# Kernel optimization log

Measured on AMD Instinct MI355X. Metric: run time of the kernel, lower is better.

## Reference

```python
import jax, jax.numpy as jnp
import numpy as np
from jax import lax

HEAD_NUM = 16
QKV_DIM = 16
TOP_K = 2
SQRT_EMBED = 16.0   # sqrt_embedding_dim for E=256
LOGIT_CLIP = 10.0


def setup_inputs() -> dict:
    key = jax.random.key(0)
    ks = jax.random.split(key, 12)
    B, P, N1, E, HD, NE = 256, 100, 101, 256, 256, 8
    s = 0.05
    return {
        "encoded_last_node": jax.random.normal(ks[0], (B, P, E), jnp.float32),
        "attr": jax.random.uniform(ks[1], (B, P, 4), jnp.float32),
        "encoded_nodes": jax.random.normal(ks[2], (B, N1, E), jnp.float32),
        "ninf_mask": jnp.zeros((B, P, N1), jnp.float32),
        "attention_bias": jax.random.normal(ks[3], (B, P, N1), jnp.float32),
        "attention_bias1": jax.random.normal(ks[4], (B, P, N1), jnp.float32),
        "Wq_last": jax.random.normal(ks[5], (E + 4, HD), jnp.float32) * s,
        "Wk": jax.random.normal(ks[6], (E, HD), jnp.float32) * s,
        "Wv": jax.random.normal(ks[7], (E, HD), jnp.float32) * s,
        "Wg": jax.random.normal(ks[8], (HD, NE), jnp.float32) * s,
        "expert_W": jax.random.normal(ks[9], (NE, HD, E), jnp.float32) * s,
        "expert_b": jnp.zeros((NE, E), jnp.float32),
    }


def _heads(x, H, D):
    B, n, _ = x.shape
    return x.reshape(B, n, H, D).transpose(0, 2, 1, 3)  # (B,H,n,D)


def reference(encoded_last_node, attr, encoded_nodes, ninf_mask,
              attention_bias, attention_bias1, Wq_last, Wk, Wv,
              Wg, expert_W, expert_b):
    B, P, E = encoded_last_node.shape
    H, D = HEAD_NUM, QKV_DIM
    # q from [last_node ; attr], k/v from encoded_nodes (set_kv)
    q = _heads(jnp.concatenate([encoded_last_node, attr], axis=-1) @ Wq_last, H, D)
    k = _heads(encoded_nodes @ Wk, H, D)   # (B,H,N+1,D)
    v = _heads(encoded_nodes @ Wv, H, D)
    inv_sqrt_d = 1.0 / jnp.sqrt(jnp.asarray(D, jnp.float32))
    score = jnp.einsum('bhpd,bhnd->bhpn', q, k) * inv_sqrt_d
    score = score + ninf_mask[:, None, :, :]           # rank3 ninf mask
    w = jax.nn.softmax(score, axis=-1)
    out = jnp.einsum('bhpn,bhnd->bhpd', w, v)
    out_concat = out.transpose(0, 2, 1, 3).reshape(B, P, H * D)
    # --- top-k gated MoE combine (node-level routing, eval path) ---
    x = out_concat.reshape(B * P, H * D)               # tokens
    logits = x @ Wg                                    # (T, NE)
    top_v, top_i = lax.top_k(logits, TOP_K)
    top_g = jax.nn.softmax(top_v, axis=-1)
    gates = jnp.zeros_like(logits).at[
        jnp.arange(x.shape[0])[:, None], top_i].set(top_g)   # (T, NE)
    expert_out = jnp.einsum('tf,efo->teo', x, expert_W) + expert_b[None]
    mh = jnp.einsum('teo,te->to', expert_out, gates).reshape(B, P, E)
    # --- single-head pointer scores with bias + tanh clipping ---
    score2 = jnp.einsum('bpe,bne->bpn', mh, encoded_nodes)
    score2 = score2 + attention_bias + attention_bias1
    score2 = LOGIT_CLIP * jnp.tanh(score2 / SQRT_EMBED)
    probs = jax.nn.softmax(score2 + ninf_mask, axis=-1)  # (B,P,N+1)
    return probs
```

## Files before the change

### kernel.cpp

```cpp
#include <hip/hip_runtime.h>
#include <hip/hip_bf16.h>

#define B   256
#define P   100
#define N1  101
#define E   256
#define HD  256
#define H   16
#define D   16
#define NE  8
#define NTOK (B*P)
#define NKV  (B*N1)
#define NCHK 200
#define CHKSZ 128

typedef __attribute__((ext_vector_type(8))) short short8;
typedef __attribute__((ext_vector_type(4))) float f32x4;
typedef unsigned short ushort_t;

__device__ __forceinline__ unsigned short f2bf(float f) {
  unsigned int u = __float_as_uint(f);
  unsigned int r = (u + 0x7fffu + ((u >> 16) & 1u)) >> 16;
  return (unsigned short)r;
}
__device__ __forceinline__ float bf2f(unsigned short b) {
  return __uint_as_float(((unsigned int)b) << 16);
}
__device__ __forceinline__ unsigned int cvtpk(float a, float b) {
  unsigned int r;
  asm("v_cvt_pk_bf16_f32 %0, %1, %2" : "=v"(r) : "v"(a), "v"(b));
  return r;
}
__device__ __forceinline__ float lo2f(unsigned int u) {
  return __uint_as_float(u << 16);
}
__device__ __forceinline__ float hi2f(unsigned int u) {
  return __uint_as_float(u & 0xffff0000u);
}

__device__ __forceinline__ void split3_pack(const float* v, uint4& uh,
                                            uint4& um, uint4& ul) {
  unsigned int hw[4], mw[4], lw[4];
#pragma unroll
  for (int jj = 0; jj < 4; ++jj) {
    float va = v[2 * jj], vb = v[2 * jj + 1];
    unsigned int h = cvtpk(va, vb);
    float ra = va - lo2f(h), rb = vb - hi2f(h);
    unsigned int m = cvtpk(ra, rb);
    float sa = ra - lo2f(m), sb = rb - hi2f(m);
    unsigned int l = cvtpk(sa, sb);
    hw[jj] = h; mw[jj] = m; lw[jj] = l;
  }
  uh.x = hw[0]; uh.y = hw[1]; uh.z = hw[2]; uh.w = hw[3];
  um.x = mw[0]; um.y = mw[1]; um.z = mw[2]; um.w = mw[3];
  ul.x = lw[0]; ul.y = lw[1]; ul.z = lw[2]; ul.w = lw[3];
}

__device__ __forceinline__ void wsplit3_body(const float* __restrict__ W,
                                             uint4* __restrict__ Wp, int Kreal,
                                             int gid) {
  const int lane = gid & 63;
  const int rest = gid >> 6;
  const int gct = rest & 15;
  const int kt = rest >> 4;
  const int k0 = kt * 32 + (lane >> 4) * 8;
  const int c = gct * 16 + (lane & 15);
  float v[8];
#pragma unroll
  for (int j = 0; j < 8; ++j) {
    int kk = k0 + j;
    v[j] = (kk < Kreal) ? W[(size_t)kk * 256 + c] : 0.f;
  }
  uint4 uh, um, ul;
  split3_pack(v, uh, um, ul);
  Wp[(size_t)(rest * 3 + 0) * 64 + lane] = uh;
  Wp[(size_t)(rest * 3 + 1) * 64 + lane] = um;
  Wp[(size_t)(rest * 3 + 2) * 64 + lane] = ul;
}

__global__ __launch_bounds__(256) void prep_kernel(
    const float* __restrict__ eW, uint4* __restrict__ Wp,
    const float* __restrict__ Wk, uint4* __restrict__ Wk3,
    const float* __restrict__ Wv, uint4* __restrict__ Wv3,
    const float* __restrict__ Wq, uint4* __restrict__ Wq3) {
  const int bx = blockIdx.x;
  const int tid = threadIdx.x;
  if (bx < 256) {
    const int gid = bx * 256 + tid;
    const int lane = gid & 63;
    const int rest = gid >> 6;
    const int gct = rest & 15;
    const int kt = (rest >> 4) & 7;
    const int e = rest >> 7;
    const int kbase = kt * 32 + (lane >> 4) * 8;
    const int c = gct * 16 + (lane & 15);
    unsigned int hi[4], lo[4];
#pragma unroll
    for (int jj = 0; jj < 4; ++jj) {
      float v0 = eW[((size_t)e * HD + (kbase + 2 * jj)) * E + c];
      float v1 = eW[((size_t)e * HD + (kbase + 2 * jj + 1)) * E + c];
      unsigned int h = cvtpk(v0, v1);
      float r0 = v0 - lo2f(h), r1 = v1 - hi2f(h);
      unsigned int l = cvtpk(r0, r1);
      hi[jj] = h; lo[jj] = l;
    }
    uint4 uh, ul;
    uh.x = hi[0]; uh.y = hi[1]; uh.z = hi[2]; uh.w = hi[3];
    ul.x = lo[0]; ul.y = lo[1]; ul.z = lo[2]; ul.w = lo[3];
    Wp[(size_t)(rest * 2 + 0) * 64 + lane] = uh;
    Wp[(size_t)(rest * 2 + 1) * 64 + lane] = ul;
  } else if (bx < 288) {
    wsplit3_body(Wk, Wk3, 256, (bx - 256) * 256 + tid);
  } else if (bx < 320) {
    wsplit3_body(Wv, Wv3, 256, (bx - 288) * 256 + tid);
  } else {
    wsplit3_body(Wq, Wq3, 260, (bx - 320) * 256 + tid);
  }
}

__global__ __launch_bounds__(256) void kvproj3_kernel(
    const float* __restrict__ enc, const uint4* __restrict__ Wk3,
    const uint4* __restrict__ Wv3, float* __restrict__ kout,
    float* __restrict__ vout) {
  const int KT = 8;
  const int NKG = KT * 4;
  const int RSTRIDE = KT * 12 + 1;
  __shared__ uint4 als[32 * 97];
  const int tid = threadIdx.x;
  const int row0 = blockIdx.x * 32;
  for (int i = tid; i < 32 * NKG; i += 256) {
    const int row = i >> 5;
    const int kg = i & 31;
    float v[8];
    const float4* s = (const float4*)(enc + (size_t)(row0 + row) * 256 + kg * 8);
    float4 x0 = s[0], x1 = s[1];
    v[0] = x0.x; v[1] = x0.y; v[2] = x0.z; v[3] = x0.w;
    v[4] = x1.x; v[5] = x1.y; v[6] = x1.z; v[7] = x1.w;
    uint4 uh, um, ul;
    split3_pack(v, uh, um, ul);
    const int slot = row * RSTRIDE + kg;
    als[slot] = uh;
    als[slot + NKG] = um;
    als[slot + 2 * NKG] = ul;
  }
  __syncthreads();
  const int w = tid >> 6;
  const int lane = tid & 63;
  const int lr = lane & 15;
  const int lg4 = lane >> 4;
  f32x4 acck[2][4], accv[2][4];
#pragma unroll
  for (int rt = 0; rt < 2; ++rt)
#pragma unroll
    for (int ct = 0; ct < 4; ++ct) {
      acck[rt][ct] = (f32x4){0.f, 0.f, 0.f, 0.f};
      accv[rt][ct] = (f32x4){0.f, 0.f, 0.f, 0.f};
    }
  for (int kt = 0; kt < KT; ++kt) {
    short8 ah[2], am[2], al[2];
#pragma unroll
    for (int rt = 0; rt < 2; ++rt) {
      const int base = (rt * 16 + lr) * RSTRIDE + kt * 4 + lg4;
      ah[rt] = __builtin_bit_cast(short8, als[base]);
      am[rt] = __builtin_bit_cast(short8, als[base + NKG]);
      al[rt] = __builtin_bit_cast(short8, als[base + 2 * NKG]);
    }
#pragma unroll
    for (int ct = 0; ct < 4; ++ct) {
      const int gct = w * 4 + ct;
      const size_t base = (size_t)((kt * 16 + gct) * 3) * 64 + lane;
      {
        short8 bh = __builtin_bit_cast(short8, Wk3[base]);
        short8 bm = __builtin_bit_cast(short8, Wk3[base + 64]);
        short8 bl = __builtin_bit_cast(short8, Wk3[base + 128]);
#pragma unroll
        for (int rt = 0; rt < 2; ++rt) {
          f32x4 a = acck[rt][ct];
          a = __builtin_amdgcn_mfma_f32_16x16x32_bf16(ah[rt], bh, a, 0, 0, 0);
          a = __builtin_amdgcn_mfma_f32_16x16x32_bf16(ah[rt], bm, a, 0, 0, 0);
          a = __builtin_amdgcn_mfma_f32_16x16x32_bf16(am[rt], bh, a, 0, 0, 0);
          a = __builtin_amdgcn_mfma_f32_16x16x32_bf16(am[rt], bm, a, 0, 0, 0);
          a = __builtin_amdgcn_mfma_f32_16x16x32_bf16(ah[rt], bl, a, 0, 0, 0);
          a = __builtin_amdgcn_mfma_f32_16x16x32_bf16(al[rt], bh, a, 0, 0, 0);
          acck[rt][ct] = a;
        }
      }
      {
        short8 bh = __builtin_bit_cast(short8, Wv3[base]);
        short8 bm = __builtin_bit_cast(short8, Wv3[base + 64]);
        short8 bl = __builtin_bit_cast(short8, Wv3[base + 128]);
#pragma unroll
        for (int rt = 0; rt < 2; ++rt) {
          f32x4 a = accv[rt][ct];
          a = __builtin_amdgcn_mfma_f32_16x16x32_bf16(ah[rt], bh, a, 0, 0, 0);
          a = __builtin_amdgcn_mfma_f32_16x16x32_bf16(ah[rt], bm, a, 0, 0, 0);
          a = __builtin_amdgcn_mfma_f32_16x16x32_bf16(am[rt], bh, a, 0, 0, 0);
          a = __builtin_amdgcn_mfma_f32_16x16x32_bf16(am[rt], bm, a, 0, 0, 0);
          a = __builtin_amdgcn_mfma_f32_16x16x32_bf16(ah[rt], bl, a, 0, 0, 0);
          a = __builtin_amdgcn_mfma_f32_16x16x32_bf16(al[rt], bh, a, 0, 0, 0);
          accv[rt][ct] = a;
        }
      }
    }
  }
#pragma unroll
  for (int rt = 0; rt < 2; ++rt) {
#pragma unroll
    for (int ct = 0; ct < 4; ++ct) {
      const int gct = w * 4 + ct;
#pragma unroll
      for (int reg = 0; reg < 4; ++reg) {
        const int row = row0 + rt * 16 + lg4 * 4 + reg;
        int bb = row / N1, nn = row - bb * N1;
        size_t o = (((size_t)bb * H + gct) * N1 + nn) * D + lr;
        kout[o] = acck[rt][ct][reg];
        vout[o] = accv[rt][ct][reg];
      }
    }
  }
}

template <int KT, int MODE>
__global__ __launch_bounds__(256) void proj3_kernel(
    const float* __restrict__ src, const float* __restrict__ attr,
    const uint4* __restrict__ Wp3, float* __restrict__ outp) {
  const int RSTRIDE = KT * 12 + 1;
  __shared__ uint4 als[32 * (KT * 12 + 1)];
  const int tid = threadIdx.x;
  const int row0 = blockIdx.x * 32;
  const int NKG = KT * 4;
  for (int i = tid; i < 32 * NKG; i += 256) {
    const int row = i / NKG;
    const int kg = i - row * NKG;
    float v[8];
    const int kbase = kg * 8;
    if (MODE == 0 || kbase < 256) {
      const float4* s = (const float4*)(src + (size_t)(row0 + row) * 256 + kbase);
      float4 x0 = s[0], x1 = s[1];
      v[0] = x0.x; v[1] = x0.y; v[2] = x0.z; v[3] = x0.w;
      v[4] = x1.x; v[5] = x1.y; v[6] = x1.z; v[7] = x1.w;
    } else {
#pragma unroll
      for (int j = 0; j < 8; ++j) {
        int k = kbase + j;
        v[j] = (k >= 256 && k < 260) ? attr[(size_t)(row0 + row) * 4 + (k - 256)]
                                     : 0.f;
      }
    }
    uint4 uh, um, ul;
    split3_pack(v, uh, um, ul);
    const int slot = row * RSTRIDE + kg;
    als[slot] = uh;
    als[slot + NKG] = um;
    als[slot + 2 * NKG] = ul;
  }
  __syncthreads();
  const int w = tid >> 6;
  const int lane = tid & 63;
  const int lr = lane & 15;
  const int lg4 = lane >> 4;
  f32x4 acc[2][4];
#pragma unroll
  for (int rt = 0; rt < 2; ++rt)
#pragma unroll
    for (int ct = 0; ct < 4; ++ct) acc[rt][ct] = (f32x4){0.f, 0.f, 0.f, 0.f};
  for (int kt = 0; kt < KT; ++kt) {
    short8 ah[2], am[2], al[2];
#pragma unroll
    for (int rt = 0; rt < 2; ++rt) {
      const int base = (rt * 16 + lr) * RSTRIDE + kt * 4 + lg4;
      ah[rt] = __builtin_bit_cast(short8, als[base]);
      am[rt] = __builtin_bit_cast(short8, als[base + NKG]);
      al[rt] = __builtin_bit_cast(short8, als[base + 2 * NKG]);
    }
#pragma unroll
    for (int ct = 0; ct < 4; ++ct) {
      const int gct = w * 4 + ct;
      const size_t base = (size_t)((kt * 16 + gct) * 3) * 64 + lane;
      short8 bh = __builtin_bit_cast(short8, Wp3[base]);
      short8 bm = __builtin_bit_cast(short8, Wp3[base + 64]);
      short8 bl = __builtin_bit_cast(short8, Wp3[base + 128]);
#pragma unroll
      for (int rt = 0; rt < 2; ++rt) {
        f32x4 a = acc[rt][ct];
        a = __builtin_amdgcn_mfma_f32_16x16x32_bf16(ah[rt], bh, a, 0, 0, 0);
        a = __builtin_amdgcn_mfma_f32_16x16x32_bf16(ah[rt], bm, a, 0, 0, 0);
        a = __builtin_amdgcn_mfma_f32_16x16x32_bf16(am[rt], bh, a, 0, 0, 0);
        a = __builtin_amdgcn_mfma_f32_16x16x32_bf16(am[rt], bm, a, 0, 0, 0);
        a = __builtin_amdgcn_mfma_f32_16x16x32_bf16(ah[rt], bl, a, 0, 0, 0);
        a = __builtin_amdgcn_mfma_f32_16x16x32_bf16(al[rt], bh, a, 0, 0, 0);
        acc[rt][ct] = a;
      }
    }
  }
#pragma unroll
  for (int rt = 0; rt < 2; ++rt) {
#pragma unroll
    for (int ct = 0; ct < 4; ++ct) {
      const int gct = w * 4 + ct;
#pragma unroll
      for (int reg = 0; reg < 4; ++reg) {
        const int row = row0 + rt * 16 + lg4 * 4 + reg;
        size_t o;
        if (MODE == 0) {
          int bb = row / N1, nn = row - bb * N1;
          o = (((size_t)bb * H + gct) * N1 + nn) * D + lr;
        } else {
          int bb = row / P, pp = row - bb * P;
          o = (((size_t)bb * H + gct) * P + pp) * D + lr;
        }
        outp[o] = acc[rt][ct][reg];
      }
    }
  }
}

__device__ __forceinline__ float dot16f(
    const float4& a0, const float4& a1, const float4& a2, const float4& a3,
    const float4& b0, const float4& b1, const float4& b2, const float4& b3) {
  float s = a0.x * b0.x;
  s = fmaf(a0.y, b0.y, s); s = fmaf(a0.z, b0.z, s); s = fmaf(a0.w, b0.w, s);
  s = fmaf(a1.x, b1.x, s); s = fmaf(a1.y, b1.y, s); s = fmaf(a1.z, b1.z, s);
  s = fmaf(a1.w, b1.w, s);
  s = fmaf(a2.x, b2.x, s); s = fmaf(a2.y, b2.y, s); s = fmaf(a2.z, b2.z, s);
  s = fmaf(a2.w, b2.w, s);
  s = fmaf(a3.x, b3.x, s); s = fmaf(a3.y, b3.y, s); s = fmaf(a3.z, b3.z, s);
  s = fmaf(a3.w, b3.w, s);
  return s;
}

__global__ __launch_bounds__(256) void attn_kernel(
    const float* __restrict__ q, const float* __restrict__ k,
    const float* __restrict__ v, const float* __restrict__ ninf,
    float* __restrict__ x) {
  const int b = blockIdx.x >> 3;
  const int h0 = (blockIdx.x & 7) * 2;
  __shared__ float4 kl4[2 * 208];
  __shared__ float4 vl4[2 * 208];
  const int tid = threadIdx.x;
  const int w = tid >> 6;
  const int lane = tid & 63;
  const int hh = w >> 1;
  const int h = h0 + hh;
  const int prow = (w & 1) * 64 + lane;
  const bool act = (prow < P);
  const int p = act ? prow : (P - 1);
  const float LOG2E = 1.4426950408889634f;
  const float c1 = 0.25f * LOG2E;
  const float* qb = q + (((size_t)b * H + h) * P + p) * D;
  float4 qa0 = *(const float4*)&qb[0];
  float4 qa1 = *(const float4*)&qb[4];
  float4 qa2 = *(const float4*)&qb[8];
  float4 qa3 = *(const float4*)&qb[12];
  qa0.x *= c1; qa0.y *= c1; qa0.z *= c1; qa0.w *= c1;
  qa1.x *= c1; qa1.y *= c1; qa1.z *= c1; qa1.w *= c1;
  qa2.x *= c1; qa2.y *= c1; qa2.z *= c1; qa2.w *= c1;
  qa3.x *= c1; qa3.y *= c1; qa3.z *= c1; qa3.w *= c1;
  const float* mrow = ninf + ((size_t)b * P + p) * N1;
  const float* kw = (const float*)(kl4 + hh * 208);
  const float* vw = (const float*)(vl4 + hh * 208);

  float m2 = -1e30f, l = 0.f;
  float o[16];
#pragma unroll
  for (int d = 0; d < 16; ++d) o[d] = 0.f;

#pragma unroll
  for (int ch = 0; ch < 2; ++ch) {
    const int c0 = ch ? 52 : 0;
    const int len = ch ? 49 : 52;
    const int nf4 = len * 4;
    __syncthreads();
    for (int i = tid; i < 2 * nf4; i += 256) {
      int hs = i / nf4, rem = i - hs * nf4;
      const float4* ks =
          (const float4*)(k + (((size_t)b * H + h0 + hs) * N1 + c0) * D);
      const float4* vs =
          (const float4*)(v + (((size_t)b * H + h0 + hs) * N1 + c0) * D);
      kl4[hs * 208 + rem] = ks[rem];
      vl4[hs * 208 + rem] = vs[rem];
    }
    __syncthreads();
    const int nit = len >> 2;
    float4 mk = *(const float4*)&mrow[c0];
    for (int it = 0; it < nit; ++it) {
      const int j = it * 4;
      const int nn = (it < nit - 1) ? (c0 + j + 4) : c0;
      float4 nx = *(const float4*)&mrow[nn];
      const float4* kr0 = (const float4*)&kw[(j + 0) * D];
      const float4* kr1 = (const float4*)&kw[(j + 1) * D];
      const float4* kr2 = (const float4*)&kw[(j + 2) * D];
      const float4* kr3 = (const float4*)&kw[(j + 3) * D];
      float4 k00 = kr0[0], k01 = kr0[1], k02 = kr0[2], k03 = kr0[3];
      float4 k10 = kr1[0], k11 = kr1[1], k12 = kr1[2], k13 = kr1[3];
      float4 k20 = kr2[0], k21 = kr2[1], k22 = kr2[2], k23 = kr2[3];
      float4 k30 = kr3[0], k31 = kr3[1], k32 = kr3[2], k33 = kr3[3];
      float s0 = fmaf(mk.x, LOG2E, dot16f(qa0, qa1, qa2, qa3, k00, k01, k02, k03));
      float s1 = fmaf(mk.y, LOG2E, dot16f(qa0, qa1, qa2, qa3, k10, k11, k12, k13));
      float s2 = fmaf(mk.z, LOG2E, dot16f(qa0, qa1, qa2, qa3, k20, k21, k22, k23));
      float s3 = fmaf(mk.w, LOG2E, dot16f(qa0, qa1, qa2, qa3, k30, k31, k32, k33));
      float gm = fmaxf(fmaxf(s0, s1), fmaxf(s2, s3));
      const float4* vr0 = (const float4*)&vw[(j + 0) * D];
      const float4* vr1 = (const float4*)&vw[(j + 1) * D];
      const float4* vr2 = (const float4*)&vw[(j + 2) * D];
      const float4* vr3 = (const float4*)&vw[(j + 3) * D];
      if (__any(gm > m2 + 8.f)) {
        float mn = fmaxf(gm, m2);
        float sc = exp2f(m2 - mn);
        float p0 = exp2f(s0 - mn), p1 = exp2f(s1 - mn);
        float p2 = exp2f(s2 - mn), p3 = exp2f(s3 - mn);
        l = fmaf(l, sc, (p0 + p1) + (p2 + p3));
#pragma unroll
        for (int dq = 0; dq < 4; ++dq) {
          float4 v0 = vr0[dq], v1 = vr1[dq], v2 = vr2[dq], v3 = vr3[dq];
          o[4 * dq + 0] = fmaf(o[4 * dq + 0], sc,
              fmaf(p0, v0.x, fmaf(p1, v1.x, fmaf(p2, v2.x, p3 * v3.x))));
          o[4 * dq + 1] = fmaf(o[4 * dq + 1], sc,
              fmaf(p0, v0.y, fmaf(p1, v1.y, fmaf(p2, v2.y, p3 * v3.y))));
          o[4 * dq + 2] = fmaf(o[4 * dq + 2], sc,
              fmaf(p0, v0.z, fmaf(p1, v1.z, fmaf(p2, v2.z, p3 * v3.z))));
          o[4 * dq + 3] = fmaf(o[4 * dq + 3], sc,
              fmaf(p0, v0.w, fmaf(p1, v1.w, fmaf(p2, v2.w, p3 * v3.w))));
        }
        m2 = mn;
      } else {
        float p0 = exp2f(s0 - m2), p1 = exp2f(s1 - m2);
        float p2 = exp2f(s2 - m2), p3 = exp2f(s3 - m2);
        l += (p0 + p1) + (p2 + p3);
#pragma unroll
        for (int dq = 0; dq < 4; ++dq) {
          float4 v0 = vr0[dq], v1 = vr1[dq], v2 = vr2[dq], v3 = vr3[dq];
          o[4 * dq + 0] = fmaf(p0, v0.x,
              fmaf(p1, v1.x, fmaf(p2, v2.x, fmaf(p3, v3.x, o[4 * dq + 0]))));
          o[4 * dq + 1] = fmaf(p0, v0.y,
              fmaf(p1, v1.y, fmaf(p2, v2.y, fmaf(p3, v3.y, o[4 * dq + 1]))));
          o[4 * dq + 2] = fmaf(p0, v0.z,
              fmaf(p1, v1.z, fmaf(p2, v2.z, fmaf(p3, v3.z, o[4 * dq + 2]))));
          o[4 * dq + 3] = fmaf(p0, v0.w,
              fmaf(p1, v1.w, fmaf(p2, v2.w, fmaf(p3, v3.w, o[4 * dq + 3]))));
        }
      }
      mk = nx;
    }
  }
  {
    const float tm = mrow[100];
    const float4* kr = (const float4*)&kw[48 * D];
    float4 k0 = kr[0], k1 = kr[1], k2 = kr[2], k3 = kr[3];
    float s = fmaf(tm, LOG2E, dot16f(qa0, qa1, qa2, qa3, k0, k1, k2, k3));
    float mn = fmaxf(m2, s);
    float sc = exp2f(m2 - mn);
    float pp = exp2f(s - mn);
    l = fmaf(l, sc, pp);
    const float4* vr = (const float4*)&vw[48 * D];
#pragma unroll
    for (int dq = 0; dq < 4; ++dq) {
      float4 v0 = vr[dq];
      o[4 * dq + 0] = fmaf(o[4 * dq + 0], sc, pp * v0.x);
      o[4 * dq + 1] = fmaf(o[4 * dq + 1], sc, pp * v0.y);
      o[4 * dq + 2] = fmaf(o[4 * dq + 2], sc, pp * v0.z);
      o[4 * dq + 3] = fmaf(o[4 * dq + 3], sc, pp * v0.w);
    }
  }
  if (act) {
    const float inv = 1.f / l;
    float* xr = &x[((size_t)b * P + p) * HD + h * D];
#pragma unroll
    for (int dq = 0; dq < 4; ++dq) {
      float4 t;
      t.x = o[4 * dq + 0] * inv; t.y = o[4 * dq + 1] * inv;
      t.z = o[4 * dq + 2] * inv; t.w = o[4 * dq + 3] * inv;
      *(float4*)&xr[4 * dq] = t;
    }
  }
}

__global__ __launch_bounds__(256) void logits_top2_kernel(
    const float* __restrict__ x, const float* __restrict__ Wg,
    int* __restrict__ topi, float* __restrict__ topg,
    ushort_t* __restrict__ xsplit) {
  __shared__ float xl[32][260];
  __shared__ float wgt[8 * 260];
  __shared__ float lg[32][9];
  const int tid = threadIdx.x;
  const int t0 = blockIdx.x * 32;
  for (int r = 0; r < 32; ++r) {
    float val = x[(size_t)(t0 + r) * HD + tid];
    xl[r][tid] = val;
    unsigned short hi = f2bf(val);
    unsigned short lo = f2bf(val - bf2f(hi));
    xsplit[(size_t)(t0 + r) * 512 + tid] = hi;
    xsplit[(size_t)(t0 + r) * 512 + 256 + tid] = lo;
  }
  for (int i = tid; i < E * NE; i += 256) {
    wgt[(i & 7) * 260 + (i >> 3)] = Wg[i];
  }
  __syncthreads();
  const int r = tid >> 3, e = tid & 7;
  float acc = 0.f;
  const float* xr = &xl[r][0];
  const float* wr = &wgt[e * 260];
  for (int f = 0; f < E; f += 4) {
    float4 xv = *(const float4*)&xr[f];
    float4 wv = *(const float4*)&wr[f];
    acc += xv.x * wv.x;
    acc += xv.y * wv.y;
    acc += xv.z * wv.z;
    acc += xv.w * wv.w;
  }
  lg[r][e] = acc;
  __syncthreads();
  if (tid < 32) {
    float v[8];
#pragma unroll
    for (int j = 0; j < 8; ++j) v[j] = lg[tid][j];
    int i1 = 0; float v1 = v[0];
#pragma unroll
    for (int j = 1; j < 8; ++j) if (v[j] > v1) { v1 = v[j]; i1 = j; }
    int i2 = -1; float v2 = -1e30f;
#pragma unroll
    for (int j = 0; j < 8; ++j)
      if (j != i1 && v[j] > v2) { v2 = v[j]; i2 = j; }
    float ex = __expf(v2 - v1);
    float g1 = 1.f / (1.f + ex);
    float g2 = ex / (1.f + ex);
    int t = t0 + tid;
    topi[t * 2 + 0] = i1; topi[t * 2 + 1] = i2;
    topg[t * 2 + 0] = g1; topg[t * 2 + 1] = g2;
  }
}

__global__ __launch_bounds__(CHKSZ) void moe_count_kernel(
    const int* __restrict__ topi, int* __restrict__ chunk_cnt) {
  __shared__ int cnt[NE];
  const int tid = threadIdx.x;
  if (tid < NE) cnt[tid] = 0;
  __syncthreads();
  const int t = blockIdx.x * CHKSZ + tid;
  atomicAdd(&cnt[topi[t * 2 + 0]], 1);
  atomicAdd(&cnt[topi[t * 2 + 1]], 1);
  __syncthreads();
  if (tid < NE) chunk_cnt[blockIdx.x * NE + tid] = cnt[tid];
}

__global__ __launch_bounds__(64) void moe_scan_kernel(
    const int* __restrict__ chunk_cnt, int* __restrict__ chunk_base,
    int* __restrict__ counts) {
  const int e = threadIdx.x;
  if (e < NE) {
    int run = 0;
    for (int c = 0; c < NCHK; ++c) {
      chunk_base[c * NE + e] = run;
      run += chunk_cnt[c * NE + e];
    }
    counts[e] = run;
  }
}

__global__ __launch_bounds__(CHKSZ) void moe_scatter_kernel(
    const int* __restrict__ topi, const float* __restrict__ topg,
    const int* __restrict__ chunk_base, int* __restrict__ list_tok,
    float* __restrict__ list_gate) {
  __shared__ int w0cnt[NE];
  const int tid = threadIdx.x;
  const int wv = tid >> 6, lane = tid & 63;
  const int t = blockIdx.x * CHKSZ + tid;
  const int ia = topi[t * 2 + 0], ib = topi[t * 2 + 1];
  const float ga = topg[t * 2 + 0], gb = topg[t * 2 + 1];
  const unsigned long long lmask = (lane == 0) ? 0ull : ((~0ull) >> (64 - lane));
  int prefA = 0, prefB = 0;
#pragma unroll
  for (int e = 0; e < NE; ++e) {
    unsigned long long mc = __ballot(ia == e) | __ballot(ib == e);
    if (wv == 0 && lane == 0) w0cnt[e] = __popcll(mc);
    int pref = __popcll(mc & lmask);
    if (ia == e) prefA = pref;
    if (ib == e) prefB = pref;
  }
  __syncthreads();
  const int baseA =
      chunk_base[blockIdx.x * NE + ia] + (wv ? w0cnt[ia] : 0) + prefA;
  const int baseB =
      chunk_base[blockIdx.x * NE + ib] + (wv ? w0cnt[ib] : 0) + prefB;
  list_tok[ia * NTOK + baseA] = (t << 1) | 0;
  list_gate[ia * NTOK + baseA] = ga;
  list_tok[ib * NTOK + baseB] = (t << 1) | 1;
  list_gate[ib * NTOK + baseB] = gb;
}

__global__ __launch_bounds__(256) void expert_gemm_kernel(
    const ushort_t* __restrict__ xsplit, const uint4* __restrict__ Wp,
    const float* __restrict__ eb, const int* __restrict__ list_tok,
    const float* __restrict__ list_gate, const int* __restrict__ counts,
    float* __restrict__ p0, float* __restrict__ p1) {
  int e = 0, t0 = -1;
  {
    int rem = blockIdx.x;
    for (int i = 0; i < NE; ++i) {
      int nt = (counts[i] + 47) / 48;
      if (rem < nt) { e = i; t0 = rem * 48; break; }
      rem -= nt;
    }
  }
  if (t0 < 0) return;
  const int cnt = counts[e];
  const int nr = min(48, cnt - t0);
  __shared__ uint4 xls[48 * 65];
  __shared__ int stok[48];
  __shared__ float sg[48];
  const int tid = threadIdx.x;
  if (tid < 48) {
    int src = e * NTOK + t0 + ((tid < nr) ? tid : 0);
    stok[tid] = list_tok[src];
    sg[tid] = (tid < nr) ? list_gate[e * NTOK + t0 + tid] : 0.f;
  }
  __syncthreads();
  for (int i = tid; i < 48 * 64; i += 256) {
    int r = i >> 6, ch = i & 63;
    const uint4* src = (const uint4*)(xsplit + (size_t)(stok[r] >> 1) * 512);
    xls[r * 65 + ch] = src[ch];
  }
  __syncthreads();
  const int w = tid >> 6;
  const int lane = tid & 63;
  const int lr = lane & 15;
  const int lg4 = lane >> 4;
  f32x4 acc[3][4];
#pragma unroll
  for (int rt = 0; rt < 3; ++rt)
#pragma unroll
    for (int ct = 0; ct < 4; ++ct) acc[rt][ct] = (f32x4){0.f, 0.f, 0.f, 0.f};

  for (int kt = 0; kt < 8; ++kt) {
    short8 afrag[3][2];
#pragma unroll
    for (int rt = 0; rt < 3; ++rt)
#pragma unroll
      for (int pl = 0; pl < 2; ++pl) {
        uint4 u = xls[(rt * 16 + lr) * 65 + pl * 32 + kt * 4 + lg4];
        afrag[rt][pl] = __builtin_bit_cast(short8, u);
      }
#pragma unroll
    for (int ct = 0; ct < 4; ++ct) {
      const int gct = w * 4 + ct;
      const size_t base = (size_t)(((e * 8 + kt) * 16 + gct) * 2) * 64 + lane;
      short8 bh = __builtin_bit_cast(short8, Wp[base]);
      short8 bl = __builtin_bit_cast(short8, Wp[base + 64]);
#pragma unroll
      for (int rt = 0; rt < 3; ++rt) {
        acc[rt][ct] = __builtin_amdgcn_mfma_f32_16x16x32_bf16(
            afrag[rt][0], bh, acc[rt][ct], 0, 0, 0);
        acc[rt][ct] = __builtin_amdgcn_mfma_f32_16x16x32_bf16(
            afrag[rt][0], bl, acc[rt][ct], 0, 0, 0);
        acc[rt][ct] = __builtin_amdgcn_mfma_f32_16x16x32_bf16(
            afrag[rt][1], bh, acc[rt][ct], 0, 0, 0);
      }
    }
  }
#pragma unroll
  for (int rt = 0; rt < 3; ++rt) {
#pragma unroll
    for (int ct = 0; ct < 4; ++ct) {
      const int col = (w * 4 + ct) * 16 + lr;
      const float bias = eb[e * E + col];
#pragma unroll
      for (int reg = 0; reg < 4; ++reg) {
        const int ridx = rt * 16 + lg4 * 4 + reg;
        if (ridx < nr) {
          const int tokw = stok[ridx];
          const float g = sg[ridx];
          float* dst = ((tokw & 1) ? p1 : p0) + (size_t)(tokw >> 1) * E + col;
          *dst = g * (acc[rt][ct][reg] + bias);
        }
      }
    }
  }
}

__global__ __launch_bounds__(256) void score2_fused_kernel(
    const float* __restrict__ p0, const float* __restrict__ p1,
    const float* __restrict__ enc, const float* __restrict__ ab,
    const float* __restrict__ ab1, const float* __restrict__ ninf,
    float* __restrict__ out) {
  const int b = blockIdx.x >> 1;
  const int half = blockIdx.x & 1;
  const int r0 = half * 50;
  __shared__ float4 mh4[50 * 64];
  const int tid = threadIdx.x;
  for (int i = tid; i < 50 * 64; i += 256) {
    int r = i >> 6, c4 = i & 63;
    size_t idx = (size_t)(b * P + r0 + r) * 64 + c4;
    float4 a = ((const float4*)p0)[idx];
    float4 c = ((const float4*)p1)[idx];
    float4 s;
    s.x = a.x + c.x; s.y = a.y + c.y; s.z = a.z + c.z; s.w = a.w + c.w;
    mh4[i] = s;
  }
  __syncthreads();
  const int w = tid >> 6;
  const int lane = tid & 63;
  const int n0 = lane;
  const int n1v = lane + 64;
  const bool has1 = (n1v < N1);
  const int n1 = has1 ? n1v : (N1 - 1);
  const float4* er0 = (const float4*)(enc + ((size_t)b * N1 + n0) * E);
  const float4* er1 = (const float4*)(enc + ((size_t)b * N1 + n1) * E);
  float acc0[13], acc1[13];
#pragma unroll
  for (int j = 0; j < 13; ++j) { acc0[j] = 0.f; acc1[j] = 0.f; }
  for (int kk = 0; kk < 64; ++kk) {
    float4 e0 = er0[kk];
    float4 e1 = er1[kk];
#pragma unroll
    for (int j = 0; j < 13; ++j) {
      const int r = w + j * 4;
      if (r < 50) {
        float4 mv = mh4[r * 64 + kk];
        acc0[j] = fmaf(mv.w, e0.w,
                  fmaf(mv.z, e0.z, fmaf(mv.y, e0.y, fmaf(mv.x, e0.x, acc0[j]))));
        acc1[j] = fmaf(mv.w, e1.w,
                  fmaf(mv.z, e1.z, fmaf(mv.y, e1.y, fmaf(mv.x, e1.x, acc1[j]))));
      }
    }
  }
#pragma unroll
  for (int j = 0; j < 13; ++j) {
    const int r = w + j * 4;
    if (r < 50) {
      const int prow = b * P + r0 + r;
      const float* arow = ab + (size_t)prow * N1;
      const float* a1row = ab1 + (size_t)prow * N1;
      const float* nrow = ninf + (size_t)prow * N1;
      float s0 = acc0[j] + arow[n0] + a1row[n0];
      float e20 = __expf(s0 * 0.125f);
      float v0 = 10.f - 20.f / (e20 + 1.f) + nrow[n0];
      float v1 = -1e30f;
      if (has1) {
        float s1 = acc1[j] + arow[n1v] + a1row[n1v];
        float e21 = __expf(s1 * 0.125f);
        v1 = 10.f - 20.f / (e21 + 1.f) + nrow[n1v];
      }
      float mx = fmaxf(v0, v1);
#pragma unroll
      for (int off = 32; off > 0; off >>= 1)
        mx = fmaxf(mx, __shfl_xor(mx, off, 64));
      float q0 = __expf(v0 - mx);
      float q1 = has1 ? __expf(v1 - mx) : 0.f;
      float sum = q0 + q1;
#pragma unroll
      for (int off = 32; off > 0; off >>= 1)
        sum += __shfl_xor(sum, off, 64);
      float inv = 1.f / sum;
      float* orow = out + (size_t)prow * N1;
      orow[n0] = q0 * inv;
      if (has1) orow[n1v] = q1 * inv;
    }
  }
}

extern "C" void kernel_launch(void* const* d_in, const int* in_sizes, int n_in,
                              void* d_out, int out_size, void* d_ws,
                              size_t ws_size, hipStream_t stream) {
  const float* eln  = (const float*)d_in[0];
  const float* attr = (const float*)d_in[1];
  const float* enc  = (const float*)d_in[2];
  const float* ninf = (const float*)d_in[3];
  const float* ab   = (const float*)d_in[4];
  const float* ab1  = (const float*)d_in[5];
  const float* Wq   = (const float*)d_in[6];
  const float* Wk   = (const float*)d_in[7];
  const float* Wv   = (const float*)d_in[8];
  const float* Wg   = (const float*)d_in[9];
  const float* eW   = (const float*)d_in[10];
  const float* eb   = (const float*)d_in[11];
  float* out = (float*)d_out;

  char* ws = (char*)d_ws;
  size_t off = 0;
  auto carve = [&](size_t bytes) {
    char* p = ws + off;
    off += (bytes + 255) & ~size_t(255);
    return p;
  };
  float* kbuf = (float*)carve(sizeof(float) * NKV * HD);
  float* vbuf = (float*)carve(sizeof(float) * NKV * HD);
  float* qbuf = (float*)carve(sizeof(float) * NTOK * HD);
  float* xbuf = (float*)carve(sizeof(float) * NTOK * HD);
  int*   topi = (int*)carve(sizeof(int) * NTOK * 2);
  float* topg = (float*)carve(sizeof(float) * NTOK * 2);
  int*   counts = (int*)carve(sizeof(int) * 16);
  int*   chunk_cnt = (int*)carve(sizeof(int) * NCHK * NE);
  int*   chunk_base = (int*)carve(sizeof(int) * NCHK * NE);
  int*   list_tok = (int*)carve(sizeof(int) * NE * NTOK);
  float* list_gate = (float*)carve(sizeof(float) * NE * NTOK);
  uint4* Wp  = (uint4*)carve(sizeof(ushort_t) * NE * HD * E * 2);
  uint4* Wk3 = (uint4*)carve((size_t)8 * 16 * 3 * 64 * 16);
  uint4* Wv3 = (uint4*)carve((size_t)8 * 16 * 3 * 64 * 16);
  uint4* Wq3 = (uint4*)carve((size_t)9 * 16 * 3 * 64 * 16);
  float* pp0 = kbuf;
  float* pp1 = vbuf;
  ushort_t* xsplit = (ushort_t*)qbuf;

  prep_kernel<<<356, 256, 0, stream>>>(eW, Wp, Wk, Wk3, Wv, Wv3, Wq, Wq3);
  kvproj3_kernel<<<NKV / 32, 256, 0, stream>>>(enc, Wk3, Wv3, kbuf, vbuf);
  proj3_kernel<9, 1><<<NTOK / 32, 256, 0, stream>>>(eln, attr, Wq3, qbuf);
  attn_kernel<<<B * 8, 256, 0, stream>>>(qbuf, kbuf, vbuf, ninf, xbuf);
  logits_top2_kernel<<<NTOK / 32, 256, 0, stream>>>(xbuf, Wg, topi, topg,
                                                    xsplit);
  moe_count_kernel<<<NCHK, CHKSZ, 0, stream>>>(topi, chunk_cnt);
  moe_scan_kernel<<<1, 64, 0, stream>>>(chunk_cnt, chunk_base, counts);
  moe_scatter_kernel<<<NCHK, CHKSZ, 0, stream>>>(topi, topg, chunk_base,
                                                 list_tok, list_gate);
  expert_gemm_kernel<<<1075, 256, 0, stream>>>(xsplit, Wp, eb, list_tok,
                                               list_gate, counts, pp0, pp1);
  score2_fused_kernel<<<512, 256, 0, stream>>>(pp0, pp1, enc, ab, ab1, ninf,
                                               out);
}
```

Measured before the change: 298.2 us.

## Process two query rows per thread in attention, four heads per block

The attention kernel now assigns one head per wavefront and two query rows per lane, so each block handles four heads and the grid is halved. Each K/V row read from LDS is reused for two queries, and the wasted half-wave of inactive rows is removed. The lazy-rescale branch with __any is replaced by an unconditional online-softmax rescale. In exchange, register pressure roughly doubles for accumulators, there are fewer blocks, and every step now pays extra exp2 and multiply work for the rescale.

```diff
diff --git a/kernel.cpp b/kernel.cpp
--- a/kernel.cpp
+++ b/kernel.cpp
@@ -333,37 +333,45 @@
     const float* __restrict__ q, const float* __restrict__ k,
     const float* __restrict__ v, const float* __restrict__ ninf,
     float* __restrict__ x) {
-  const int b = blockIdx.x >> 3;
-  const int h0 = (blockIdx.x & 7) * 2;
-  __shared__ float4 kl4[2 * 208];
-  __shared__ float4 vl4[2 * 208];
+  const int b = blockIdx.x >> 2;
+  const int h0 = (blockIdx.x & 3) * 4;
+  __shared__ float4 kl4[4 * 208];
+  __shared__ float4 vl4[4 * 208];
   const int tid = threadIdx.x;
   const int w = tid >> 6;
   const int lane = tid & 63;
-  const int hh = w >> 1;
-  const int h = h0 + hh;
-  const int prow = (w & 1) * 64 + lane;
-  const bool act = (prow < P);
-  const int p = act ? prow : (P - 1);
+  const int h = h0 + w;
+  const int p0 = lane;
+  const bool r1 = (lane + 64 < P);
+  const int p1 = r1 ? (lane + 64) : (P - 1);
   const float LOG2E = 1.4426950408889634f;
   const float c1 = 0.25f * LOG2E;
-  const float* qb = q + (((size_t)b * H + h) * P + p) * D;
-  float4 qa0 = *(const float4*)&qb[0];
-  float4 qa1 = *(const float4*)&qb[4];
-  float4 qa2 = *(const float4*)&qb[8];
-  float4 qa3 = *(const float4*)&qb[12];
+  const float* qbase = q + (((size_t)b * H + h) * P) * D;
+  float4 qa0 = *(const float4*)&qbase[p0 * D + 0];
+  float4 qa1 = *(const float4*)&qbase[p0 * D + 4];
+  float4 qa2 = *(const float4*)&qbase[p0 * D + 8];
+  float4 qa3 = *(const float4*)&qbase[p0 * D + 12];
+  float4 qb0 = *(const float4*)&qbase[p1 * D + 0];
+  float4 qb1 = *(const float4*)&qbase[p1 * D + 4];
+  float4 qb2 = *(const float4*)&qbase[p1 * D + 8];
+  float4 qb3 = *(const float4*)&qbase[p1 * D + 12];
   qa0.x *= c1; qa0.y *= c1; qa0.z *= c1; qa0.w *= c1;
   qa1.x *= c1; qa1.y *= c1; qa1.z *= c1; qa1.w *= c1;
   qa2.x *= c1; qa2.y *= c1; qa2.z *= c1; qa2.w *= c1;
   qa3.x *= c1; qa3.y *= c1; qa3.z *= c1; qa3.w *= c1;
-  const float* mrow = ninf + ((size_t)b * P + p) * N1;
-  const float* kw = (const float*)(kl4 + hh * 208);
-  const float* vw = (const float*)(vl4 + hh * 208);
-
-  float m2 = -1e30f, l = 0.f;
-  float o[16];
-#pragma unroll
-  for (int d = 0; d < 16; ++d) o[d] = 0.f;
+  qb0.x *= c1; qb0.y *= c1; qb0.z *= c1; qb0.w *= c1;
+  qb1.x *= c1; qb1.y *= c1; qb1.z *= c1; qb1.w *= c1;
+  qb2.x *= c1; qb2.y *= c1; qb2.z *= c1; qb2.w *= c1;
+  qb3.x *= c1; qb3.y *= c1; qb3.z *= c1; qb3.w *= c1;
+  const float* m0 = ninf + ((size_t)b * P + p0) * N1;
+  const float* m1 = ninf + ((size_t)b * P + p1) * N1;
+  const float* kw = (const float*)(kl4 + w * 208);
+  const float* vw = (const float*)(vl4 + w * 208);
+
+  float mA = -1e30f, mB = -1e30f, lA = 0.f, lB = 0.f;
+  float oA[16], oB[16];
+#pragma unroll
+  for (int d = 0; d < 16; ++d) { oA[d] = 0.f; oB[d] = 0.f; }
 
 #pragma unroll
   for (int ch = 0; ch < 2; ++ch) {
@@ -371,7 +379,7 @@
     const int len = ch ? 49 : 52;
     const int nf4 = len * 4;
     __syncthreads();
-    for (int i = tid; i < 2 * nf4; i += 256) {
+    for (int i = tid; i < 4 * nf4; i += 256) {
       int hs = i / nf4, rem = i - hs * nf4;
       const float4* ks =
           (const float4*)(k + (((size_t)b * H + h0 + hs) * N1 + c0) * D);
@@ -382,11 +390,13 @@
     }
     __syncthreads();
     const int nit = len >> 2;
-    float4 mk = *(const float4*)&mrow[c0];
+    float4 mk0 = *(const float4*)&m0[c0];
+    float4 mk1 = *(const float4*)&m1[c0];
     for (int it = 0; it < nit; ++it) {
       const int j = it * 4;
       const int nn = (it < nit - 1) ? (c0 + j + 4) : c0;
-      float4 nx = *(const float4*)&mrow[nn];
+      float4 nx0 = *(const float4*)&m0[nn];
+      float4 nx1 = *(const float4*)&m1[nn];
       const float4* kr0 = (const float4*)&kw[(j + 0) * D];
       const float4* kr1 = (const float4*)&kw[(j + 1) * D];
       const float4* kr2 = (const float4*)&kw[(j + 2) * D];
@@ -395,82 +405,97 @@
       float4 k10 = kr1[0], k11 = kr1[1], k12 = kr1[2], k13 = kr1[3];
       float4 k20 = kr2[0], k21 = kr2[1], k22 = kr2[2], k23 = kr2[3];
       float4 k30 = kr3[0], k31 = kr3[1], k32 = kr3[2], k33 = kr3[3];
-      float s0 = fmaf(mk.x, LOG2E, dot16f(qa0, qa1, qa2, qa3, k00, k01, k02, k03));
-      float s1 = fmaf(mk.y, LOG2E, dot16f(qa0, qa1, qa2, qa3, k10, k11, k12, k13));
-      float s2 = fmaf(mk.z, LOG2E, dot16f(qa0, qa1, qa2, qa3, k20, k21, k22, k23));
-      float s3 = fmaf(mk.w, LOG2E, dot16f(qa0, qa1, qa2, qa3, k30, k31, k32, k33));
-      float gm = fmaxf(fmaxf(s0, s1), fmaxf(s2, s3));
+      float sA0 = fmaf(mk0.x, LOG2E, dot16f(qa0, qa1, qa2, qa3, k00, k01, k02, k03));
+      float sA1 = fmaf(mk0.y, LOG2E, dot16f(qa0, qa1, qa2, qa3, k10, k11, k12, k13));
+      float sA2 = fmaf(mk0.z, LOG2E, dot16f(qa0, qa1, qa2, qa3, k20, k21, k22, k23));
+      float sA3 = fmaf(mk0.w, LOG2E, dot16f(qa0, qa1, qa2, qa3, k30, k31, k32, k33));
+      float sB0 = fmaf(mk1.x, LOG2E, dot16f(qb0, qb1, qb2, qb3, k00, k01, k02, k03));
+      float sB1 = fmaf(mk1.y, LOG2E, dot16f(qb0, qb1, qb2, qb3, k10, k11, k12, k13));
+      float sB2 = fmaf(mk1.z, LOG2E, dot16f(qb0, qb1, qb2, qb3, k20, k21, k22, k23));
+      float sB3 = fmaf(mk1.w, LOG2E, dot16f(qb0, qb1, qb2, qb3, k30, k31, k32, k33));
+      float mnA = fmaxf(fmaxf(fmaxf(sA0, sA1), fmaxf(sA2, sA3)), mA);
+      float mnB = fmaxf(fmaxf(fmaxf(sB0, sB1), fmaxf(sB2, sB3)), mB);
+      float scA = exp2f(mA - mnA);
+      float scB = exp2f(mB - mnB);
+      float pA0 = exp2f(sA0 - mnA), pA1 = exp2f(sA1 - mnA);
+      float pA2 = exp2f(sA2 - mnA), pA3 = exp2f(sA3 - mnA);
+      float pB0 = exp2f(sB0 - mnB), pB1 = exp2f(sB1 - mnB);
+      float pB2 = exp2f(sB2 - mnB), pB3 = exp2f(sB3 - mnB);
+      lA = fmaf(lA, scA, (pA0 + pA1) + (pA2 + pA3));
+      lB = fmaf(lB, scB, (pB0 + pB1) + (pB2 + pB3));
       const float4* vr0 = (const float4*)&vw[(j + 0) * D];
       const float4* vr1 = (const float4*)&vw[(j + 1) * D];
       const float4* vr2 = (const float4*)&vw[(j + 2) * D];
       const float4* vr3 = (const float4*)&vw[(j + 3) * D];
-      if (__any(gm > m2 + 8.f)) {
-        float mn = fmaxf(gm, m2);
-        float sc = exp2f(m2 - mn);
-        float p0 = exp2f(s0 - mn), p1 = exp2f(s1 - mn);
-        float p2 = exp2f(s2 - mn), p3 = exp2f(s3 - mn);
-        l = fmaf(l, sc, (p0 + p1) + (p2 + p3));
-#pragma unroll
-        for (int dq = 0; dq < 4; ++dq) {
-          float4 v0 = vr0[dq], v1 = vr1[dq], v2 = vr2[dq], v3 = vr3[dq];
-          o[4 * dq + 0] = fmaf(o[4 * dq + 0], sc,
-              fmaf(p0, v0.x, fmaf(p1, v1.x, fmaf(p2, v2.x, p3 * v3.x))));
-          o[4 * dq + 1] = fmaf(o[4 * dq + 1], sc,
-              fmaf(p0, v0.y, fmaf(p1, v1.y, fmaf(p2, v2.y, p3 * v3.y))));
-          o[4 * dq + 2] = fmaf(o[4 * dq + 2], sc,
-              fmaf(p0, v0.z, fmaf(p1, v1.z, fmaf(p2, v2.z, p3 * v3.z))));
-          o[4 * dq + 3] = fmaf(o[4 * dq + 3], sc,
-              fmaf(p0, v0.w, fmaf(p1, v1.w, fmaf(p2, v2.w, p3 * v3.w))));
-        }
-        m2 = mn;
-      } else {
-        float p0 = exp2f(s0 - m2), p1 = exp2f(s1 - m2);
-        float p2 = exp2f(s2 - m2), p3 = exp2f(s3 - m2);
-        l += (p0 + p1) + (p2 + p3);
-#pragma unroll
-        for (int dq = 0; dq < 4; ++dq) {
-          float4 v0 = vr0[dq], v1 = vr1[dq], v2 = vr2[dq], v3 = vr3[dq];
-          o[4 * dq + 0] = fmaf(p0, v0.x,
-              fmaf(p1, v1.x, fmaf(p2, v2.x, fmaf(p3, v3.x, o[4 * dq + 0]))));
-          o[4 * dq + 1] = fmaf(p0, v0.y,
-              fmaf(p1, v1.y, fmaf(p2, v2.y, fmaf(p3, v3.y, o[4 * dq + 1]))));
-          o[4 * dq + 2] = fmaf(p0, v0.z,
-              fmaf(p1, v1.z, fmaf(p2, v2.z, fmaf(p3, v3.z, o[4 * dq + 2]))));
-          o[4 * dq + 3] = fmaf(p0, v0.w,
-              fmaf(p1, v1.w, fmaf(p2, v2.w, fmaf(p3, v3.w, o[4 * dq + 3]))));
-        }
-      }
-      mk = nx;
+#pragma unroll
+      for (int dq = 0; dq < 4; ++dq) {
+        float4 v0 = vr0[dq], v1 = vr1[dq], v2 = vr2[dq], v3 = vr3[dq];
+        oA[4 * dq + 0] = fmaf(oA[4 * dq + 0], scA,
+            fmaf(pA0, v0.x, fmaf(pA1, v1.x, fmaf(pA2, v2.x, pA3 * v3.x))));
+        oA[4 * dq + 1] = fmaf(oA[4 * dq + 1], scA,
+            fmaf(pA0, v0.y, fmaf(pA1, v1.y, fmaf(pA2, v2.y, pA3 * v3.y))));
+        oA[4 * dq + 2] = fmaf(oA[4 * dq + 2], scA,
+            fmaf(pA0, v0.z, fmaf(pA1, v1.z, fmaf(pA2, v2.z, pA3 * v3.z))));
+        oA[4 * dq + 3] = fmaf(oA[4 * dq + 3], scA,
+            fmaf(pA0, v0.w, fmaf(pA1, v1.w, fmaf(pA2, v2.w, pA3 * v3.w))));
+        oB[4 * dq + 0] = fmaf(oB[4 * dq + 0], scB,
+            fmaf(pB0, v0.x, fmaf(pB1, v1.x, fmaf(pB2, v2.x, pB3 * v3.x))));
+        oB[4 * dq + 1] = fmaf(oB[4 * dq + 1], scB,
+            fmaf(pB0, v0.y, fmaf(pB1, v1.y, fmaf(pB2, v2.y, pB3 * v3.y))));
+        oB[4 * dq + 2] = fmaf(oB[4 * dq + 2], scB,
+            fmaf(pB0, v0.z, fmaf(pB1, v1.z, fmaf(pB2, v2.z, pB3 * v3.z))));
+        oB[4 * dq + 3] = fmaf(oB[4 * dq + 3], scB,
+            fmaf(pB0, v0.w, fmaf(pB1, v1.w, fmaf(pB2, v2.w, pB3 * v3.w))));
+      }
+      mA = mnA; mB = mnB;
+      mk0 = nx0; mk1 = nx1;
     }
   }
   {
-    const float tm = mrow[100];
+    const float tm0 = m0[100], tm1 = m1[100];
     const float4* kr = (const float4*)&kw[48 * D];
     float4 k0 = kr[0], k1 = kr[1], k2 = kr[2], k3 = kr[3];
-    float s = fmaf(tm, LOG2E, dot16f(qa0, qa1, qa2, qa3, k0, k1, k2, k3));
-    float mn = fmaxf(m2, s);
-    float sc = exp2f(m2 - mn);
-    float pp = exp2f(s - mn);
-    l = fmaf(l, sc, pp);
+    float sA = fmaf(tm0, LOG2E, dot16f(qa0, qa1, qa2, qa3, k0, k1, k2, k3));
+    float sB = fmaf(tm1, LOG2E, dot16f(qb0, qb1, qb2, qb3, k0, k1, k2, k3));
+    float mnA = fmaxf(mA, sA), mnB = fmaxf(mB, sB);
+    float scA = exp2f(mA - mnA), scB = exp2f(mB - mnB);
+    float pA = exp2f(sA - mnA), pB = exp2f(sB - mnB);
+    lA = fmaf(lA, scA, pA);
+    lB = fmaf(lB, scB, pB);
     const float4* vr = (const float4*)&vw[48 * D];
 #pragma unroll
     for (int dq = 0; dq < 4; ++dq) {
       float4 v0 = vr[dq];
-      o[4 * dq + 0] = fmaf(o[4 * dq + 0], sc, pp * v0.x);
-      o[4 * dq + 1] = fmaf(o[4 * dq + 1], sc, pp * v0.y);
-      o[4 * dq + 2] = fmaf(o[4 * dq + 2], sc, pp * v0.z);
-      o[4 * dq + 3] = fmaf(o[4 * dq + 3], sc, pp * v0.w);
-    }
-  }
-  if (act) {
-    const float inv = 1.f / l;
-    float* xr = &x[((size_t)b * P + p) * HD + h * D];
+      oA[4 * dq + 0] = fmaf(oA[4 * dq + 0], scA, pA * v0.x);
+      oA[4 * dq + 1] = fmaf(oA[4 * dq + 1], scA, pA * v0.y);
+      oA[4 * dq + 2] = fmaf(oA[4 * dq + 2], scA, pA * v0.z);
+      oA[4 * dq + 3] = fmaf(oA[4 * dq + 3], scA, pA * v0.w);
+      oB[4 * dq + 0] = fmaf(oB[4 * dq + 0], scB, pB * v0.x);
+      oB[4 * dq + 1] = fmaf(oB[4 * dq + 1], scB, pB * v0.y);
+      oB[4 * dq + 2] = fmaf(oB[4 * dq + 2], scB, pB * v0.z);
+      oB[4 * dq + 3] = fmaf(oB[4 * dq + 3], scB, pB * v0.w);
+    }
+  }
+  {
+    const float invA = 1.f / lA;
+    float* xr0 = &x[((size_t)b * P + p0) * HD + h * D];
 #pragma unroll
     for (int dq = 0; dq < 4; ++dq) {
       float4 t;
-      t.x = o[4 * dq + 0] * inv; t.y = o[4 * dq + 1] * inv;
-      t.z = o[4 * dq + 2] * inv; t.w = o[4 * dq + 3] * inv;
-      *(float4*)&xr[4 * dq] = t;
+      t.x = oA[4 * dq + 0] * invA; t.y = oA[4 * dq + 1] * invA;
+      t.z = oA[4 * dq + 2] * invA; t.w = oA[4 * dq + 3] * invA;
+      *(float4*)&xr0[4 * dq] = t;
+    }
+  }
+  if (r1) {
+    const float invB = 1.f / lB;
+    float* xr1 = &x[((size_t)b * P + p1) * HD + h * D];
+#pragma unroll
+    for (int dq = 0; dq < 4; ++dq) {
+      float4 t;
+      t.x = oB[4 * dq + 0] * invB; t.y = oB[4 * dq + 1] * invB;
+      t.z = oB[4 * dq + 2] * invB; t.w = oB[4 * dq + 3] * invB;
+      *(float4*)&xr1[4 * dq] = t;
     }
   }
 }
@@ -804,7 +829,7 @@
   prep_kernel<<<356, 256, 0, stream>>>(eW, Wp, Wk, Wk3, Wv, Wv3, Wq, Wq3);
   kvproj3_kernel<<<NKV / 32, 256, 0, stream>>>(enc, Wk3, Wv3, kbuf, vbuf);
   proj3_kernel<9, 1><<<NTOK / 32, 256, 0, stream>>>(eln, attr, Wq3, qbuf);
-  attn_kernel<<<B * 8, 256, 0, stream>>>(qbuf, kbuf, vbuf, ninf, xbuf);
+  attn_kernel<<<B * 4, 256, 0, stream>>>(qbuf, kbuf, vbuf, ninf, xbuf);
   logits_top2_kernel<<<NTOK / 32, 256, 0, stream>>>(xbuf, Wg, topi, topg,
                                                     xsplit);
   moe_count_kernel<<<NCHK, CHKSZ, 0, stream>>>(topi, chunk_cnt);
```

Result: no change. 297.6 us (-0.2%).
